# Performance work log

Hardware: AMD Instinct MI355X
Metric: run time of the kernel (lower is better)

## Reference

```python
import jax, jax.numpy as jnp
import numpy as np

B, T, C, S = 16, 32768, 64, 4  # batch, time, channels, n_sections


def setup_inputs() -> dict:
    key = jax.random.key(0)
    x = jax.random.normal(key, (B, T, C), dtype=jnp.float32)
    # Build STABLE biquad sections (random coeffs would blow up over 32k steps).
    rng = np.random.default_rng(0)
    r = rng.uniform(0.5, 0.9, S)                      # pole radius < 1 -> stable
    th = rng.uniform(0.1, np.pi - 0.1, S)             # pole angle
    a1 = -2.0 * r * np.cos(th)
    a2 = r ** 2
    b = rng.normal(0.0, 0.5, (S, 3))
    sos = np.concatenate([b, np.stack([np.ones(S), a1, a2], axis=1)], axis=1)
    return {"x": x, "sos": jnp.asarray(sos, dtype=jnp.float32)}


def _biquad(sig, b, a):
    # sig: [N, T]; direct-form-I recurrence, exactly the math of lfilter_bg with n_order=3:
    b0, b1, b2 = b[0], b[1], b[2]
    a0, a1, a2 = a[0], a[1], a[2]

    def step(carry, xt):
        x1, x2, y1, y2 = carry
        y = (b0 * xt + b1 * x1 + b2 * x2 - a1 * y1 - a2 * y2) / a0
        return (xt, x1, y, y1), y

    z = jnp.zeros((sig.shape[0],), sig.dtype)
    _, ys = jax.lax.scan(step, (z, z, z, z), sig.T)  # scan over time -> ys [T, N]
    return ys.T


def reference(x, sos):
    # x: [B, T, C] -> transpose(1,2) -> [B, C, T]; lfilter_bg flattens leading dims.
    Bb, Tt, Cc = x.shape
    sig = jnp.transpose(x, (0, 2, 1)).reshape(Bb * Cc, Tt)
    for s in range(sos.shape[0]):  # small fixed cascade of sections
        sig = _biquad(sig, sos[s, :3], sos[s, 3:])
    return jnp.transpose(sig.reshape(Bb, Cc, Tt), (0, 2, 1))
```

## Files before the change

### kernel.cpp

```cpp
#include <hip/hip_runtime.h>


#define TLEN  32768
#define CCH   64
#define BATCH 16
#define NSEC  4
#define CHUNK 128
#define WARM  120
#define SKEW  3

#define NCHUNKS (TLEN / CHUNK)
#define NWAVES  (BATCH * NCHUNKS)
#define BLOCK   256
#define NBLOCKS (NWAVES * 64 / BLOCK)

#define ISSUE(NB, G) do {                                                     \
    int rb_ = s0 + 8 * (G);                                                   \
    rb_ = (rb_ > TLEN - 8) ? (TLEN - 8) : rb_;                                \
    const float* __restrict__ p_ = xb + (size_t)rb_ * CCH;                    \
    NB[0] = p_[0 * CCH]; NB[1] = p_[1 * CCH];                                 \
    NB[2] = p_[2 * CCH]; NB[3] = p_[3 * CCH];                                 \
    NB[4] = p_[4 * CCH]; NB[5] = p_[5 * CCH];                                 \
    NB[6] = p_[6 * CCH]; NB[7] = p_[7 * CCH];                                 \
} while (0)

#define STEP(CB, j, ps, SB, SE) do {                                          \
    const float i0 = CB[j], i1 = lat1, i2 = lat2, i3 = lat3;                  \
    const float p0 = fmaf(cb0[0], i0, fmaf(cb1[0], x1[0], cb2[0] * x2[0]));   \
    const float p1 = fmaf(cb0[1], i1, fmaf(cb1[1], x1[1], cb2[1] * x2[1]));   \
    const float p2 = fmaf(cb0[2], i2, fmaf(cb1[2], x1[2], cb2[2] * x2[2]));   \
    const float p3 = fmaf(cb0[3], i3, fmaf(cb1[3], x1[3], cb2[3] * x2[3]));   \
    const float o0 = fmaf(ca1[0], y1v[0], fmaf(ca2[0], y2v[0], p0));          \
    const float o1 = fmaf(ca1[1], y1v[1], fmaf(ca2[1], y2v[1], p1));          \
    const float o2 = fmaf(ca1[2], y1v[2], fmaf(ca2[2], y2v[2], p2));          \
    const float o3 = fmaf(ca1[3], y1v[3], fmaf(ca2[3], y2v[3], p3));          \
    x2[0] = x1[0]; x1[0] = i0;  y2v[0] = y1v[0]; y1v[0] = o0;                 \
    x2[1] = x1[1]; x1[1] = i1;  y2v[1] = y1v[1]; y1v[1] = o1;                 \
    x2[2] = x1[2]; x1[2] = i2;  y2v[2] = y1v[2]; y1v[2] = o2;                 \
    x2[3] = x1[3]; x1[3] = i3;  y2v[3] = y1v[3]; y1v[3] = o3;                 \
    lat1 = o0; lat2 = o1; lat3 = o2;                                          \
    if ((j) >= (SB) && (j) < (SE)) ps[(j) * CCH] = o3;                        \
} while (0)

#define GROUP(CB, NB, G, H, SB, SE) do {                                      \
    ISSUE(NB, (G) + 2);                                                       \
    float* __restrict__ ps = py + (ptrdiff_t)(8 * (H) - 3) * CCH;             \
    STEP(CB, 0, ps, SB, SE); STEP(CB, 1, ps, SB, SE);                         \
    STEP(CB, 2, ps, SB, SE); STEP(CB, 3, ps, SB, SE);                         \
    STEP(CB, 4, ps, SB, SE); STEP(CB, 5, ps, SB, SE);                         \
    STEP(CB, 6, ps, SB, SE); STEP(CB, 7, ps, SB, SE);                         \
} while (0)

__global__ __launch_bounds__(BLOCK, 4) void sos_kernel(const float* __restrict__ x,
                                                       const float* __restrict__ sos,
                                                       float* __restrict__ out) {
    const int lane = threadIdx.x & 63;
    const int wid  = __builtin_amdgcn_readfirstlane(
                         blockIdx.x * (BLOCK >> 6) + (threadIdx.x >> 6));
    const int b    = wid >> 8;
    const int k    = wid & (NCHUNKS - 1);
    const int t0   = k * CHUNK;
    const int warm = k ? WARM : 0;
    const int s0   = t0 - warm;

    const float* __restrict__ xb = x + (size_t)b * TLEN * CCH + lane;
    float* __restrict__ py = out + ((size_t)b * TLEN + (size_t)t0) * CCH + lane;

    float Af[8], Bf[8], Cf[8];
    ISSUE(Af, 0);
    ISSUE(Bf, 1);

    float cb0[NSEC], cb1[NSEC], cb2[NSEC], ca1[NSEC], ca2[NSEC];
    float x1[NSEC], x2[NSEC], y1v[NSEC], y2v[NSEC];
#pragma unroll
    for (int s = 0; s < NSEC; ++s) {
        const float inva = 1.0f / sos[s * 6 + 3];
        cb0[s] =  sos[s * 6 + 0] * inva;
        cb1[s] =  sos[s * 6 + 1] * inva;
        cb2[s] =  sos[s * 6 + 2] * inva;
        ca1[s] = -sos[s * 6 + 4] * inva;
        ca2[s] = -sos[s * 6 + 5] * inva;
        x1[s] = x2[s] = y1v[s] = y2v[s] = 0.0f;
    }
    float lat1 = 0.0f, lat2 = 0.0f, lat3 = 0.0f;

    int g = 0;
    if (warm) {
#pragma unroll 1
        for (int t = 0; t < 5; ++t) {
            GROUP(Af, Cf, g + 0, 0, 0, 0);
            GROUP(Bf, Af, g + 1, 0, 0, 0);
            GROUP(Cf, Bf, g + 2, 0, 0, 0);
            g += 3;
        }
    }
    GROUP(Af, Cf, g, 0, 3, 8); ++g;
#pragma unroll 1
    for (int t = 0; t < 5; ++t) {
        GROUP(Bf, Af, g + 0, 3 * t + 1, 0, 8);
        GROUP(Cf, Bf, g + 1, 3 * t + 2, 0, 8);
        GROUP(Af, Cf, g + 2, 3 * t + 3, 0, 8);
        g += 3;
    }
    {
        float* __restrict__ ps = py + (ptrdiff_t)(8 * 16 - 3) * CCH;
        STEP(Bf, 0, ps, 0, 3);
        STEP(Bf, 1, ps, 0, 3);
        STEP(Bf, 2, ps, 0, 3);
    }
}

extern "C" void kernel_launch(void* const* d_in, const int* in_sizes, int n_in,
                              void* d_out, int out_size, void* d_ws, size_t ws_size,
                              hipStream_t stream) {
    const float* x   = (const float*)d_in[0];
    const float* sos = (const float*)d_in[1];
    float* out = (float*)d_out;
    sos_kernel<<<NBLOCKS, BLOCK, 0, stream>>>(x, sos, out);
}
```

Baseline: 251.1 us.

## Stage input via async global-to-LDS loads, halve chunk, flush outputs as float4

Input rows are now brought in with global_load_lds into a per-wave 4-slot LDS ring, with explicit vmcnt waits, instead of per-lane scalar register loads. The output of the last biquad section is staged in LDS and written out as float4 stores rather than one scalar store per lane per step. Chunk length drops from 128 to 64 with a 96-sample warm-up, which doubles the number of waves and raises parallelism but makes the redundant warm-up a larger share of the work. The hand-placed vmcnt counts and the skewed index bookkeeping are fragile, and the ring-slot reuse could race if any count is wrong.

```diff
diff --git a/kernel.cpp b/kernel.cpp
--- a/kernel.cpp
+++ b/kernel.cpp
@@ -5,27 +5,33 @@
 #define CCH   64
 #define BATCH 16
 #define NSEC  4
-#define CHUNK 128
-#define WARM  120
-#define SKEW  3
+#define CHUNK 64
+#define WARM  96
 
 #define NCHUNKS (TLEN / CHUNK)
 #define NWAVES  (BATCH * NCHUNKS)
 #define BLOCK   256
 #define NBLOCKS (NWAVES * 64 / BLOCK)
 
-#define ISSUE(NB, G) do {                                                     \
+#define GLL(gp, lp)                                                           \
+    __builtin_amdgcn_global_load_lds(                                         \
+        (const __attribute__((address_space(1))) void*)(gp),                  \
+        (__attribute__((address_space(3))) void*)(lp), 16, 0, 0)
+
+#define WAITV_IMPL(N) asm volatile("s_waitcnt vmcnt(" #N ")" ::: "memory")
+#define WAITV(N) WAITV_IMPL(N)
+
+#define ISSUE(G, lp) do {                                                     \
     int rb_ = s0 + 8 * (G);                                                   \
-    rb_ = (rb_ > TLEN - 8) ? (TLEN - 8) : rb_;                                \
-    const float* __restrict__ p_ = xb + (size_t)rb_ * CCH;                    \
-    NB[0] = p_[0 * CCH]; NB[1] = p_[1 * CCH];                                 \
-    NB[2] = p_[2 * CCH]; NB[3] = p_[3 * CCH];                                 \
-    NB[4] = p_[4 * CCH]; NB[5] = p_[5 * CCH];                                 \
-    NB[6] = p_[6 * CCH]; NB[7] = p_[7 * CCH];                                 \
+    rb_ = rb_ < 0 ? 0 : rb_;                                                  \
+    rb_ = rb_ > TLEN - 8 ? TLEN - 8 : rb_;                                    \
+    const float* gp_ = xb4 + (size_t)rb_ * CCH + (lane << 2);                 \
+    GLL(gp_, (lp));                                                           \
+    GLL(gp_ + 256, (lp) + 256);                                               \
 } while (0)
 
-#define STEP(CB, j, ps, SB, SE) do {                                          \
-    const float i0 = CB[j], i1 = lat1, i2 = lat2, i3 = lat3;                  \
+#define FBODY(xin)                                                            \
+    const float i0 = (xin), i1 = lat1, i2 = lat2, i3 = lat3;                  \
     const float p0 = fmaf(cb0[0], i0, fmaf(cb1[0], x1[0], cb2[0] * x2[0]));   \
     const float p1 = fmaf(cb0[1], i1, fmaf(cb1[1], x1[1], cb2[1] * x2[1]));   \
     const float p2 = fmaf(cb0[2], i2, fmaf(cb1[2], x1[2], cb2[2] * x2[2]));   \
@@ -38,37 +44,78 @@
     x2[1] = x1[1]; x1[1] = i1;  y2v[1] = y1v[1]; y1v[1] = o1;                 \
     x2[2] = x1[2]; x1[2] = i2;  y2v[2] = y1v[2]; y1v[2] = o2;                 \
     x2[3] = x1[3]; x1[3] = i3;  y2v[3] = y1v[3]; y1v[3] = o3;                 \
-    lat1 = o0; lat2 = o1; lat3 = o2;                                          \
-    if ((j) >= (SB) && (j) < (SE)) ps[(j) * CCH] = o3;                        \
+    lat1 = o0; lat2 = o1; lat3 = o2;
+
+#define STEP_NS(xin)            do { FBODY(xin); (void)o3; } while (0)
+#define STEP_STAGE(xin, SL, q)  do { FBODY(xin); ring[(SL)*512 + (q)*64 + lane] = o3; } while (0)
+#define STEP_DW(xin, r)         do { FBODY(xin); po[(size_t)(r) * CCH] = o3; } while (0)
+
+#define FLUSH4(SL, q0, r0) do {                                               \
+    const float4 v_ = *(const float4*)&ring[(SL)*512 + (q0)*64 + lane*4];     \
+    *(float4*)&pq[(size_t)(r0) * CCH] = v_;                                   \
 } while (0)
 
-#define GROUP(CB, NB, G, H, SB, SE) do {                                      \
-    ISSUE(NB, (G) + 2);                                                       \
-    float* __restrict__ ps = py + (ptrdiff_t)(8 * (H) - 3) * CCH;             \
-    STEP(CB, 0, ps, SB, SE); STEP(CB, 1, ps, SB, SE);                         \
-    STEP(CB, 2, ps, SB, SE); STEP(CB, 3, ps, SB, SE);                         \
-    STEP(CB, 4, ps, SB, SE); STEP(CB, 5, ps, SB, SE);                         \
-    STEP(CB, 6, ps, SB, SE); STEP(CB, 7, ps, SB, SE);                         \
+#define READ8(SL)                                                             \
+    xr[0] = ring[(SL)*512 + 0*64 + lane];                                     \
+    xr[1] = ring[(SL)*512 + 1*64 + lane];                                     \
+    xr[2] = ring[(SL)*512 + 2*64 + lane];                                     \
+    xr[3] = ring[(SL)*512 + 3*64 + lane];                                     \
+    xr[4] = ring[(SL)*512 + 4*64 + lane];                                     \
+    xr[5] = ring[(SL)*512 + 5*64 + lane];                                     \
+    xr[6] = ring[(SL)*512 + 6*64 + lane];                                     \
+    xr[7] = ring[(SL)*512 + 7*64 + lane];
+
+#define WGROUP(u, g) do {                                                     \
+    ISSUE((g) + 3, ring + (((u) + 3) & 3) * 512);                             \
+    WAITV(6);                                                                 \
+    float xr[8];                                                              \
+    READ8(u);                                                                 \
+    const float wm_ = (s0 + 8 * (g) >= 0) ? 1.0f : 0.0f;                      \
+    STEP_NS(xr[0] * wm_); STEP_NS(xr[1] * wm_);                               \
+    STEP_NS(xr[2] * wm_); STEP_NS(xr[3] * wm_);                               \
+    STEP_NS(xr[4] * wm_); STEP_NS(xr[5] * wm_);                               \
+    STEP_NS(xr[6] * wm_); STEP_NS(xr[7] * wm_);                               \
+} while (0)
+
+#define SGROUP(G, SL, SLI, NW, r0) do {                                       \
+    ISSUE((G) + 3, ring + (SLI) * 512);                                       \
+    WAITV(NW);                                                                \
+    float xr[8];                                                              \
+    READ8(SL);                                                                \
+    STEP_STAGE(xr[0], SL, 0); STEP_STAGE(xr[1], SL, 1);                       \
+    STEP_STAGE(xr[2], SL, 2); STEP_STAGE(xr[3], SL, 3);                       \
+    STEP_STAGE(xr[4], SL, 4); STEP_STAGE(xr[5], SL, 5);                       \
+    STEP_STAGE(xr[6], SL, 6); STEP_STAGE(xr[7], SL, 7);                       \
+    FLUSH4(SL, 0, r0); FLUSH4(SL, 4, (r0) + 4);                               \
+} while (0)
+
+#define SGROUP_NOPF(G, SL, NW, r0) do {                                       \
+    WAITV(NW);                                                                \
+    float xr[8];                                                              \
+    READ8(SL);                                                                \
+    STEP_STAGE(xr[0], SL, 0); STEP_STAGE(xr[1], SL, 1);                       \
+    STEP_STAGE(xr[2], SL, 2); STEP_STAGE(xr[3], SL, 3);                       \
+    STEP_STAGE(xr[4], SL, 4); STEP_STAGE(xr[5], SL, 5);                       \
+    STEP_STAGE(xr[6], SL, 6); STEP_STAGE(xr[7], SL, 7);                       \
+    FLUSH4(SL, 0, r0); FLUSH4(SL, 4, (r0) + 4);                               \
 } while (0)
 
 __global__ __launch_bounds__(BLOCK, 4) void sos_kernel(const float* __restrict__ x,
                                                        const float* __restrict__ sos,
                                                        float* __restrict__ out) {
+    __shared__ alignas(16) float smem[4 * 4 * 512];
     const int lane = threadIdx.x & 63;
-    const int wid  = __builtin_amdgcn_readfirstlane(
-                         blockIdx.x * (BLOCK >> 6) + (threadIdx.x >> 6));
-    const int b    = wid >> 8;
+    const int warp = threadIdx.x >> 6;
+    const int wid  = __builtin_amdgcn_readfirstlane(blockIdx.x * (BLOCK >> 6) + warp);
+    const int b    = wid >> 9;
     const int k    = wid & (NCHUNKS - 1);
     const int t0   = k * CHUNK;
-    const int warm = k ? WARM : 0;
-    const int s0   = t0 - warm;
+    const int s0   = t0 - WARM;
 
-    const float* __restrict__ xb = x + (size_t)b * TLEN * CCH + lane;
-    float* __restrict__ py = out + ((size_t)b * TLEN + (size_t)t0) * CCH + lane;
-
-    float Af[8], Bf[8], Cf[8];
-    ISSUE(Af, 0);
-    ISSUE(Bf, 1);
+    float* __restrict__ ring = smem + warp * 2048;
+    const float* __restrict__ xb4 = x + (size_t)b * TLEN * CCH;
+    float* __restrict__ po = out + ((size_t)b * TLEN + t0) * CCH + lane;
+    float* __restrict__ pq = out + ((size_t)b * TLEN + t0) * CCH + lane * 4;
 
     float cb0[NSEC], cb1[NSEC], cb2[NSEC], ca1[NSEC], ca2[NSEC];
     float x1[NSEC], x2[NSEC], y1v[NSEC], y2v[NSEC];
@@ -84,29 +131,48 @@
     }
     float lat1 = 0.0f, lat2 = 0.0f, lat3 = 0.0f;
 
-    int g = 0;
-    if (warm) {
+    asm volatile("" ::: "memory");
+
+    ISSUE(0, ring + 0 * 512);
+    ISSUE(1, ring + 1 * 512);
+    ISSUE(2, ring + 2 * 512);
+
 #pragma unroll 1
-        for (int t = 0; t < 5; ++t) {
-            GROUP(Af, Cf, g + 0, 0, 0, 0);
-            GROUP(Bf, Af, g + 1, 0, 0, 0);
-            GROUP(Cf, Bf, g + 2, 0, 0, 0);
-            g += 3;
-        }
+    for (int t = 0; t < 12; t += 4) {
+        WGROUP(0, t + 0);
+        WGROUP(1, t + 1);
+        WGROUP(2, t + 2);
+        WGROUP(3, t + 3);
     }
-    GROUP(Af, Cf, g, 0, 3, 8); ++g;
-#pragma unroll 1
-    for (int t = 0; t < 5; ++t) {
-        GROUP(Bf, Af, g + 0, 3 * t + 1, 0, 8);
-        GROUP(Cf, Bf, g + 1, 3 * t + 2, 0, 8);
-        GROUP(Af, Cf, g + 2, 3 * t + 3, 0, 8);
-        g += 3;
+
+    {
+        ISSUE(15, ring + 3 * 512);
+        WAITV(6);
+        float xr[8];
+        READ8(0);
+        STEP_NS(xr[0]); STEP_NS(xr[1]); STEP_NS(xr[2]);
+        STEP_STAGE(xr[3], 0, 3); STEP_STAGE(xr[4], 0, 4);
+        STEP_STAGE(xr[5], 0, 5); STEP_STAGE(xr[6], 0, 6);
+        STEP_DW(xr[7], 4);
+        FLUSH4(0, 3, 0);
     }
+
+    SGROUP(13, 1, 0, 8,  5);
+    SGROUP(14, 2, 1, 10, 13);
+    SGROUP(15, 3, 2, 12, 21);
+    SGROUP(16, 0, 3, 12, 29);
+    SGROUP(17, 1, 0, 12, 37);
+    SGROUP_NOPF(18, 2, 10, 45);
+    SGROUP_NOPF(19, 3, 8, 53);
+
     {
-        float* __restrict__ ps = py + (ptrdiff_t)(8 * 16 - 3) * CCH;
-        STEP(Bf, 0, ps, 0, 3);
-        STEP(Bf, 1, ps, 0, 3);
-        STEP(Bf, 2, ps, 0, 3);
+        WAITV(6);
+        float xr0 = ring[0 * 512 + 0 * 64 + lane];
+        float xr1 = ring[0 * 512 + 1 * 64 + lane];
+        float xr2 = ring[0 * 512 + 2 * 64 + lane];
+        STEP_DW(xr0, 61);
+        STEP_DW(xr1, 62);
+        STEP_DW(xr2, 63);
     }
 }
 
```

Result: faster. 244.2 us (-2.7%).

## Halve chunk size, buffer outputs in registers, and fully unroll straight-line filter

Applied to the files above, without the earlier changes.

Chunks shrink from 128 to 64 time steps with a 96-step warmup instead of 120, doubling the number of waves so more independent recurrences run at once. The kernel becomes fully unrolled straight-line code with no loops or per-chunk-0 branch. Chunk 0 instead feeds a zero-masked, clamped warmup. Outputs are held in a 64-entry register array and stored at the end rather than interleaved with the recurrence. In exchange, redundant warmup work rises relative to useful work, register pressure grows at the launch bound, and the shorter warmup may lower accuracy.

```diff
diff --git a/kernel.cpp b/kernel.cpp
--- a/kernel.cpp
+++ b/kernel.cpp
@@ -3,20 +3,19 @@
 
 #define TLEN  32768
 #define CCH   64
-#define BATCH 16
 #define NSEC  4
-#define CHUNK 128
-#define WARM  120
-#define SKEW  3
+#define CHUNK 64
+#define WARM  96
 
 #define NCHUNKS (TLEN / CHUNK)
-#define NWAVES  (BATCH * NCHUNKS)
+#define NWAVES  (16 * NCHUNKS)
 #define BLOCK   256
 #define NBLOCKS (NWAVES * 64 / BLOCK)
 
 #define ISSUE(NB, G) do {                                                     \
     int rb_ = s0 + 8 * (G);                                                   \
-    rb_ = (rb_ > TLEN - 8) ? (TLEN - 8) : rb_;                                \
+    rb_ = rb_ < 0 ? 0 : rb_;                                                  \
+    rb_ = rb_ > TLEN - 8 ? TLEN - 8 : rb_;                                    \
     const float* __restrict__ p_ = xb + (size_t)rb_ * CCH;                    \
     NB[0] = p_[0 * CCH]; NB[1] = p_[1 * CCH];                                 \
     NB[2] = p_[2 * CCH]; NB[3] = p_[3 * CCH];                                 \
@@ -24,8 +23,8 @@
     NB[6] = p_[6 * CCH]; NB[7] = p_[7 * CCH];                                 \
 } while (0)
 
-#define STEP(CB, j, ps, SB, SE) do {                                          \
-    const float i0 = CB[j], i1 = lat1, i2 = lat2, i3 = lat3;                  \
+#define FBODY(xin)                                                            \
+    const float i0 = (xin), i1 = lat1, i2 = lat2, i3 = lat3;                  \
     const float p0 = fmaf(cb0[0], i0, fmaf(cb1[0], x1[0], cb2[0] * x2[0]));   \
     const float p1 = fmaf(cb0[1], i1, fmaf(cb1[1], x1[1], cb2[1] * x2[1]));   \
     const float p2 = fmaf(cb0[2], i2, fmaf(cb1[2], x1[2], cb2[2] * x2[2]));   \
@@ -38,17 +37,26 @@
     x2[1] = x1[1]; x1[1] = i1;  y2v[1] = y1v[1]; y1v[1] = o1;                 \
     x2[2] = x1[2]; x1[2] = i2;  y2v[2] = y1v[2]; y1v[2] = o2;                 \
     x2[3] = x1[3]; x1[3] = i3;  y2v[3] = y1v[3]; y1v[3] = o3;                 \
-    lat1 = o0; lat2 = o1; lat3 = o2;                                          \
-    if ((j) >= (SB) && (j) < (SE)) ps[(j) * CCH] = o3;                        \
+    lat1 = o0; lat2 = o1; lat3 = o2;
+
+#define STEP_NS(xin)    do { FBODY(xin); (void)o3; } while (0)
+#define STEP_Y(xin, R)  do { FBODY(xin); yout[R] = o3; } while (0)
+
+#define WG(CB, NB, g) do {                                                    \
+    ISSUE(NB, (g) + 2);                                                       \
+    const float wm_ = (s0 + 8 * (g) >= 0) ? 1.0f : 0.0f;                      \
+    STEP_NS(CB[0] * wm_); STEP_NS(CB[1] * wm_);                               \
+    STEP_NS(CB[2] * wm_); STEP_NS(CB[3] * wm_);                               \
+    STEP_NS(CB[4] * wm_); STEP_NS(CB[5] * wm_);                               \
+    STEP_NS(CB[6] * wm_); STEP_NS(CB[7] * wm_);                               \
 } while (0)
 
-#define GROUP(CB, NB, G, H, SB, SE) do {                                      \
-    ISSUE(NB, (G) + 2);                                                       \
-    float* __restrict__ ps = py + (ptrdiff_t)(8 * (H) - 3) * CCH;             \
-    STEP(CB, 0, ps, SB, SE); STEP(CB, 1, ps, SB, SE);                         \
-    STEP(CB, 2, ps, SB, SE); STEP(CB, 3, ps, SB, SE);                         \
-    STEP(CB, 4, ps, SB, SE); STEP(CB, 5, ps, SB, SE);                         \
-    STEP(CB, 6, ps, SB, SE); STEP(CB, 7, ps, SB, SE);                         \
+#define SG(CB, NB, g, R0) do {                                                \
+    ISSUE(NB, (g) + 2);                                                       \
+    STEP_Y(CB[0], (R0) + 0); STEP_Y(CB[1], (R0) + 1);                         \
+    STEP_Y(CB[2], (R0) + 2); STEP_Y(CB[3], (R0) + 3);                         \
+    STEP_Y(CB[4], (R0) + 4); STEP_Y(CB[5], (R0) + 5);                         \
+    STEP_Y(CB[6], (R0) + 6); STEP_Y(CB[7], (R0) + 7);                         \
 } while (0)
 
 __global__ __launch_bounds__(BLOCK, 4) void sos_kernel(const float* __restrict__ x,
@@ -57,14 +65,13 @@
     const int lane = threadIdx.x & 63;
     const int wid  = __builtin_amdgcn_readfirstlane(
                          blockIdx.x * (BLOCK >> 6) + (threadIdx.x >> 6));
-    const int b    = wid >> 8;
+    const int b    = wid >> 9;
     const int k    = wid & (NCHUNKS - 1);
     const int t0   = k * CHUNK;
-    const int warm = k ? WARM : 0;
-    const int s0   = t0 - warm;
+    const int s0   = t0 - WARM;
 
     const float* __restrict__ xb = x + (size_t)b * TLEN * CCH + lane;
-    float* __restrict__ py = out + ((size_t)b * TLEN + (size_t)t0) * CCH + lane;
+    float* __restrict__ py = out + ((size_t)b * TLEN + t0) * CCH + lane;
 
     float Af[8], Bf[8], Cf[8];
     ISSUE(Af, 0);
@@ -84,29 +91,39 @@
     }
     float lat1 = 0.0f, lat2 = 0.0f, lat3 = 0.0f;
 
-    int g = 0;
-    if (warm) {
-#pragma unroll 1
-        for (int t = 0; t < 5; ++t) {
-            GROUP(Af, Cf, g + 0, 0, 0, 0);
-            GROUP(Bf, Af, g + 1, 0, 0, 0);
-            GROUP(Cf, Bf, g + 2, 0, 0, 0);
-            g += 3;
-        }
+    float yout[64];
+
+    WG(Af, Cf, 0);  WG(Bf, Af, 1);  WG(Cf, Bf, 2);
+    WG(Af, Cf, 3);  WG(Bf, Af, 4);  WG(Cf, Bf, 5);
+    WG(Af, Cf, 6);  WG(Bf, Af, 7);  WG(Cf, Bf, 8);
+    WG(Af, Cf, 9);  WG(Bf, Af, 10); WG(Cf, Bf, 11);
+
+    {
+        ISSUE(Cf, 14);
+        STEP_NS(Af[0]); STEP_NS(Af[1]); STEP_NS(Af[2]);
+        STEP_Y(Af[3], 0); STEP_Y(Af[4], 1); STEP_Y(Af[5], 2);
+        STEP_Y(Af[6], 3); STEP_Y(Af[7], 4);
     }
-    GROUP(Af, Cf, g, 0, 3, 8); ++g;
-#pragma unroll 1
-    for (int t = 0; t < 5; ++t) {
-        GROUP(Bf, Af, g + 0, 3 * t + 1, 0, 8);
-        GROUP(Cf, Bf, g + 1, 3 * t + 2, 0, 8);
-        GROUP(Af, Cf, g + 2, 3 * t + 3, 0, 8);
-        g += 3;
+
+    SG(Bf, Af, 13, 5);
+    SG(Cf, Bf, 14, 13);
+    SG(Af, Cf, 15, 21);
+    SG(Bf, Af, 16, 29);
+    SG(Cf, Bf, 17, 37);
+    SG(Af, Cf, 18, 45);
+
+    {
+        STEP_Y(Bf[0], 53); STEP_Y(Bf[1], 54); STEP_Y(Bf[2], 55);
+        STEP_Y(Bf[3], 56); STEP_Y(Bf[4], 57); STEP_Y(Bf[5], 58);
+        STEP_Y(Bf[6], 59); STEP_Y(Bf[7], 60);
     }
     {
-        float* __restrict__ ps = py + (ptrdiff_t)(8 * 16 - 3) * CCH;
-        STEP(Bf, 0, ps, 0, 3);
-        STEP(Bf, 1, ps, 0, 3);
-        STEP(Bf, 2, ps, 0, 3);
+        STEP_Y(Cf[0], 61); STEP_Y(Cf[1], 62); STEP_Y(Cf[2], 63);
+    }
+
+#pragma unroll
+    for (int r = 0; r < 64; ++r) {
+        py[(size_t)r * CCH] = yout[r];
     }
 }
 
```

After: 243.3 us. 1.03x faster.
